# Optimization experiments

Hardware: AMD Instinct MI355X
Metric: run time of the kernel (lower is better)

The kernel has to match this reference:

```python
import jax, jax.numpy as jnp
import numpy as np

E = 4       # num_edge_types
DEPTH = 3   # args.depth (weight_tying=False -> DEPTH message layers)
V = 117     # num_atom_types


def setup_inputs() -> dict:
    key = jax.random.key(0)
    ks = jax.random.split(key, 13)
    mb, atoms, D, M = 1024, 128, 256, 512
    s = 0.05  # weight scale
    return {
        "atom_array": jax.random.randint(ks[0], (mb, atoms), 0, V),
        "adj": jax.random.uniform(ks[1], (mb, E, atoms, atoms), dtype=jnp.float32),
        "embed": jax.random.normal(ks[2], (V, D), jnp.float32) * s,
        "msg_W": jax.random.normal(ks[3], (DEPTH, E * D, D), jnp.float32) * s,
        "msg_b": jnp.zeros((DEPTH, E * D), jnp.float32),
        "W_ih": jax.random.normal(ks[4], (3 * D, D), jnp.float32) * s,
        "b_ih": jnp.zeros((3 * D,), jnp.float32),
        "W_hh": jax.random.normal(ks[5], (3 * D, D), jnp.float32) * s,
        "b_hh": jnp.zeros((3 * D,), jnp.float32),
        "i_W": jax.random.normal(ks[6], (M, 2 * D), jnp.float32) * s,
        "i_b": jnp.zeros((M,), jnp.float32),
        "j_W": jax.random.normal(ks[7], (M, D), jnp.float32) * s,
        "j_b": jnp.zeros((M,), jnp.float32),
    }


def _gru_cell(x, h, W_ih, b_ih, W_hh, b_hh):
    # PyTorch GRUCell math. x: input (message), h: hidden state.
    gi = x @ W_ih.T + b_ih
    gh = h @ W_hh.T + b_hh
    ir, iz, in_ = jnp.split(gi, 3, axis=-1)
    hr, hz, hn = jnp.split(gh, 3, axis=-1)
    r = jax.nn.sigmoid(ir + hr)
    z = jax.nn.sigmoid(iz + hz)
    n = jnp.tanh(in_ + r * hn)
    return (1.0 - z) * n + z * h


def reference(atom_array, adj, embed, msg_W, msg_b, W_ih, b_ih, W_hh, b_hh, i_W, i_b, j_W, j_b):
    mb, atoms = atom_array.shape
    D = embed.shape[1]
    h = embed[atom_array]          # [mb, atoms, D]
    h0 = h
    for step in range(DEPTH):
        # message: Linear(D -> E*D) then per-edge-type adjacency bmm, summed over edge types
        m = h @ msg_W[step].T + msg_b[step]            # [mb, atoms, E*D]
        m = m.reshape(mb, atoms, E, D).transpose(0, 2, 1, 3)  # [mb, E, atoms, D]
        m = jnp.einsum('beij,bejd->bid', adj, m)       # bmm + sum over edge types
        hid = h if step > 0 else jnp.zeros_like(h)     # GRUCell(hidden=None) at step 0
        h = _gru_cell(m, hid, W_ih, b_ih, W_hh, b_hh)  # [mb, atoms, D]
    # gated readout
    gate = jax.nn.sigmoid(jnp.concatenate([h, h0], axis=-1) @ i_W.T + i_b)  # [mb, atoms, M]
    val = h @ j_W.T + j_b                                                    # [mb, atoms, M]
    return jnp.sum(gate * val, axis=1)                                       # [mb, M]
```

## Files before the change

kernel.cpp:

```cpp
#include <hip/hip_runtime.h>
#include <cstdint>
#include <cstddef>

using f32x4 = float __attribute__((ext_vector_type(4)));
using u16x8 = unsigned short __attribute__((ext_vector_type(8)));
using u16x4 = unsigned short __attribute__((ext_vector_type(4)));
typedef _Float16 f16x8 __attribute__((ext_vector_type(8)));

#define DEV static __device__ __forceinline__

DEV unsigned short f2h(float f) {
  _Float16 x = (_Float16)f;
  return __builtin_bit_cast(unsigned short, x);
}
DEV float h2f(unsigned short s) {
  return (float)__builtin_bit_cast(_Float16, s);
}
DEV float sigm(float x) { return 1.f / (1.f + __expf(-x)); }
DEV float tanh_(float x) { return 2.f / (1.f + __expf(-2.f * x)) - 1.f; }

#define MFMA_F16(acc, va, vb) \
  acc = __builtin_amdgcn_mfma_f32_16x16x32_f16(va, vb, acc, 0, 0, 0)

constexpr int NB = 1024;
constexpr int AT = 128;
constexpr int DD = 256;
constexpr int MOUT = 512;
constexpr long NR = (long)NB * AT;

#define VWAIT(n) do { asm volatile("s_waitcnt vmcnt(" #n ")" ::: "memory"); \
                      __builtin_amdgcn_sched_barrier(0); } while (0)
#define LWAIT do { asm volatile("s_waitcnt lgkmcnt(0)" ::: "memory"); \
                   __builtin_amdgcn_sched_barrier(0); } while (0)
#define BARR do { __builtin_amdgcn_sched_barrier(0); __builtin_amdgcn_s_barrier(); \
                  __builtin_amdgcn_sched_barrier(0); } while (0)

#define XCD_SWZ(WG, N) const int WG = ((int)blockIdx.x & 7) * ((N) / 8) + ((int)blockIdx.x >> 3);

__global__ __launch_bounds__(256) void k_cvt(const float* __restrict__ src,
                                             unsigned short* __restrict__ dst) {
  long base = ((long)blockIdx.x * 256 + threadIdx.x) * 8;
  f32x4 v0 = *(const f32x4*)(src + base);
  f32x4 v1 = *(const f32x4*)(src + base + 4);
  u16x8 o;
  #pragma unroll
  for (int q = 0; q < 4; ++q) o[q] = f2h(v0[q]);
  #pragma unroll
  for (int q = 0; q < 4; ++q) o[4 + q] = f2h(v1[q]);
  *(u16x8*)(dst + base) = o;
}

__global__ __launch_bounds__(256) void k_cvt5(const float* __restrict__ s0, unsigned short* __restrict__ d0,
                                              const float* __restrict__ s1, unsigned short* __restrict__ d1,
                                              const float* __restrict__ s2, unsigned short* __restrict__ d2,
                                              const float* __restrict__ s3, unsigned short* __restrict__ d3,
                                              const float* __restrict__ s4, unsigned short* __restrict__ d4) {
  int blk = blockIdx.x;
  const float* s; unsigned short* d;
  if (blk < 384)      { s = s0; d = d0; }
  else if (blk < 480) { s = s1; d = d1; blk -= 384; }
  else if (blk < 576) { s = s2; d = d2; blk -= 480; }
  else if (blk < 704) { s = s3; d = d3; blk -= 576; }
  else                { s = s4; d = d4; blk -= 704; }
  long base = ((long)blk * 256 + threadIdx.x) * 8;
  f32x4 v0 = *(const f32x4*)(s + base);
  f32x4 v1 = *(const f32x4*)(s + base + 4);
  u16x8 o;
  #pragma unroll
  for (int q = 0; q < 4; ++q) o[q] = f2h(v0[q]);
  #pragma unroll
  for (int q = 0; q < 4; ++q) o[4 + q] = f2h(v1[q]);
  *(u16x8*)(d + base) = o;
}

__global__ __launch_bounds__(256) void k_gather(const int* __restrict__ atom,
                                                const float* __restrict__ embed,
                                                unsigned short* __restrict__ h,
                                                unsigned short* __restrict__ h0) {
  long idx = (long)blockIdx.x * 256 + threadIdx.x;
  long n = idx >> 6;
  int ch = (int)(idx & 63);
  int a = atom[n];
  f32x4 v = *(const f32x4*)(embed + (size_t)a * DD + ch * 4);
  u16x4 o;
  #pragma unroll
  for (int q = 0; q < 4; ++q) o[q] = f2h(v[q]);
  *(u16x4*)(h  + n * DD + ch * 4) = o;
  *(u16x4*)(h0 + n * DD + ch * 4) = o;
}

#define GEMM_IDS \
  const int tid = threadIdx.x, lane = tid & 63, wave = tid >> 6; \
  const int wr = wave >> 1, wc = wave & 1; \
  const int l15 = lane & 15, lg = lane >> 4; \
  const int sseg = (l15 >> 1) & 3;

#define GLDS(SRC, STRIDE, DST) \
  { \
    _Pragma("unroll") \
    for (int j_ = 0; j_ < 2; ++j_) { \
      const unsigned short* g_ = (SRC) + \
          (size_t)((wave * 2 + j_) * 16 + (lane >> 2)) * (STRIDE) + \
          ((lane & 3) ^ ((lane >> 3) & 3)) * 8; \
      __builtin_amdgcn_global_load_lds( \
          (const __attribute__((address_space(1))) void*)g_, \
          (__attribute__((address_space(3))) void*)&DST[(wave * 2 + j_) * 16][0], \
          16, 0, 0); \
    } \
  }

#define GLDS64(SRC, STRIDE, DST) \
  { \
    const unsigned short* g_ = (SRC) + \
        (size_t)(wave * 16 + (lane >> 2)) * (STRIDE) + \
        ((lane & 3) ^ ((lane >> 3) & 3)) * 8; \
    __builtin_amdgcn_global_load_lds( \
        (const __attribute__((address_space(1))) void*)g_, \
        (__attribute__((address_space(3))) void*)&DST[wave * 16][0], \
        16, 0, 0); \
  }

#define LOAD_A(AH) \
  f16x8 ah[4]; \
  _Pragma("unroll") \
  for (int m_ = 0; m_ < 4; ++m_) \
    ah[m_] = *(const f16x8*)&AH[wr * 64 + m_ * 16 + l15][(lg ^ sseg) * 8];

#define LOAD_B(BH) \
  f16x8 bh[4]; \
  _Pragma("unroll") \
  for (int n_ = 0; n_ < 4; ++n_) \
    bh[n_] = *(const f16x8*)&BH[wc * 64 + n_ * 16 + l15][(lg ^ sseg) * 8];

#define MFMA_TILE(ACC) \
  _Pragma("unroll") \
  for (int m_ = 0; m_ < 4; ++m_) \
    _Pragma("unroll") \
    for (int n_ = 0; n_ < 4; ++n_) \
      MFMA_F16(ACC[m_][n_], ah[m_], bh[n_]);

__global__ __launch_bounds__(256) void k_msgadj(const unsigned short* __restrict__ h,
                                                const unsigned short* __restrict__ W,
                                                const float* __restrict__ bias,
                                                const unsigned short* __restrict__ adjh,
                                                unsigned short* __restrict__ m_out) {
  __shared__ __align__(16) char pool[16384 + 128 * 136 * 2];
  typedef unsigned short row32[32];
  row32* As_[2] = { (row32*)pool,          (row32*)(pool + 16384) };
  row32* Bs_[2] = { (row32*)(pool + 8192), (row32*)(pool + 24576) };
  unsigned short (*PT)[136] = (unsigned short (*)[136])(pool + 16384);
  GEMM_IDS
  XCD_SWZ(wg, 2048)
  const size_t b = wg >> 1;
  const int d0 = (wg & 1) * 128;
  const unsigned short* hb = h + (size_t)b * 128 * 256;
  const unsigned short* adjb = adjh + (size_t)b * 4 * 128 * 128;
  f32x4 accM[4][4] = {};
  for (int e = 0; e < 4; ++e) {
    f32x4 accP[4][4] = {};
    const unsigned short* We = W + (size_t)(e * 256 + d0) * 256;
    const unsigned short* adje = adjb + (size_t)e * 128 * 128;
    GLDS(hb, 256, As_[0])
    GLDS(We, 256, Bs_[0])
    #pragma unroll
    for (int k0i = 0; k0i < 8; ++k0i) {
      const int cur = k0i & 1;
      if (k0i < 7) {
        row32* an_ = As_[cur ^ 1];
        row32* bn_ = Bs_[cur ^ 1];
        GLDS(hb + (k0i + 1) * 32, 256, an_)
        GLDS(We + (k0i + 1) * 32, 256, bn_)
      } else {
        GLDS(adje + 0 * 32, 128, As_[0])
        GLDS(adje + 1 * 32, 128, Bs_[0])
      }
      VWAIT(4);
      BARR;
      {
        row32* ac_ = As_[cur];
        row32* bc_ = Bs_[cur];
        LOAD_A(ac_)
        LOAD_B(bc_)
        MFMA_TILE(accP)
      }
      BARR;
    }
    #pragma unroll
    for (int m_ = 0; m_ < 4; ++m_) {
      int j0 = wr * 64 + m_ * 16 + lg * 4;
      #pragma unroll
      for (int n_ = 0; n_ < 4; ++n_) {
        int c = wc * 64 + n_ * 16 + l15;
        float bb = bias[e * 256 + d0 + c];
        u16x4 o;
        #pragma unroll
        for (int q = 0; q < 4; ++q) o[q] = f2h(accP[m_][n_][q] + bb);
        *(u16x4*)&PT[c][j0] = o;
      }
    }
    LWAIT;
    BARR;
    #pragma unroll
    for (int kt = 0; kt < 4; ++kt) {
      if (kt == 1) { GLDS(adje + 2 * 32, 128, As_[0]) }
      if (kt == 2) { GLDS(adje + 3 * 32, 128, Bs_[0]) }
      if (kt < 3) { VWAIT(2); } else { VWAIT(0); }
      BARR;
      {
        row32* ac_ = (kt & 1) ? Bs_[0] : As_[0];
        LOAD_A(ac_)
        f16x8 bh[4];
        #pragma unroll
        for (int n_ = 0; n_ < 4; ++n_)
          bh[n_] = *(const f16x8*)&PT[wc * 64 + n_ * 16 + l15][kt * 32 + lg * 8];
        MFMA_TILE(accM)
      }
      BARR;
    }
  }
  #pragma unroll
  for (int m_ = 0; m_ < 4; ++m_) {
    int i0 = wr * 64 + m_ * 16 + lg * 4;
    #pragma unroll
    for (int n_ = 0; n_ < 4; ++n_) {
      int c = d0 + wc * 64 + n_ * 16 + l15;
      #pragma unroll
      for (int q = 0; q < 4; ++q)
        m_out[((size_t)b * 128 + i0 + q) * 256 + c] = f2h(accM[m_][n_][q]);
    }
  }
}

template <bool HAS_H>
__global__ __launch_bounds__(256) void k_grufuse(const unsigned short* __restrict__ m,
                                                 const unsigned short* __restrict__ h,
                                                 const unsigned short* __restrict__ wih,
                                                 const unsigned short* __restrict__ whh,
                                                 const float* __restrict__ b_ih,
                                                 const float* __restrict__ b_hh,
                                                 unsigned short* __restrict__ h_new) {
  __shared__ unsigned short As[3][64][32];
  __shared__ unsigned short Br[3][64][32], Bz[3][64][32], Bn[3][64][32];
  GEMM_IDS
  XCD_SWZ(wg, 8192)
  const size_t b = wg >> 3;
  const int quad = wg & 7;
  const int r0 = (quad >> 2) * 64;
  const int c0 = (quad & 3) * 64;
  const unsigned short* msrc = m + ((size_t)b * 128 + r0) * 256;
  const unsigned short* hsrc = h + ((size_t)b * 128 + r0) * 256;
  constexpr int NKT = HAS_H ? 16 : 8;

  f32x4 accR[2][2] = {}, accZ[2][2] = {}, accI[2][2] = {}, accN[2][2] = {};

  auto stage = [&](int t, int s) {
    const unsigned short* a_ = ((HAS_H && t >= 8) ? hsrc : msrc) + (t & 7) * 32;
    const unsigned short* w_ = (HAS_H && t >= 8) ? whh : wih;
    GLDS64(a_, 256, As[s])
    GLDS64(w_ + (size_t)(c0) * 256 + (t & 7) * 32, 256, Br[s])
    GLDS64(w_ + (size_t)(256 + c0) * 256 + (t & 7) * 32, 256, Bz[s])
    GLDS64(w_ + (size_t)(512 + c0) * 256 + (t & 7) * 32, 256, Bn[s])
  };

  stage(0, 0);
  stage(1, 1);
  #pragma unroll
  for (int kt = 0; kt < NKT; ++kt) {
    const int cur = kt % 3;
    if (kt + 2 < NKT) stage(kt + 2, (kt + 2) % 3);
    if (kt + 2 < NKT) { VWAIT(8); } else if (kt + 2 == NKT) { VWAIT(4); } else { VWAIT(0); }
    BARR;
    f16x8 af[2], brf[2], bzf[2], bnf[2];
    #pragma unroll
    for (int m_ = 0; m_ < 2; ++m_)
      af[m_] = *(const f16x8*)&As[cur][wr * 32 + m_ * 16 + l15][(lg ^ sseg) * 8];
    #pragma unroll
    for (int n_ = 0; n_ < 2; ++n_) {
      brf[n_] = *(const f16x8*)&Br[cur][wc * 32 + n_ * 16 + l15][(lg ^ sseg) * 8];
      bzf[n_] = *(const f16x8*)&Bz[cur][wc * 32 + n_ * 16 + l15][(lg ^ sseg) * 8];
      bnf[n_] = *(const f16x8*)&Bn[cur][wc * 32 + n_ * 16 + l15][(lg ^ sseg) * 8];
    }
    #pragma unroll
    for (int m_ = 0; m_ < 2; ++m_)
      #pragma unroll
      for (int n_ = 0; n_ < 2; ++n_) {
        MFMA_F16(accR[m_][n_], af[m_], brf[n_]);
        MFMA_F16(accZ[m_][n_], af[m_], bzf[n_]);
        if (!HAS_H || kt < 8) { MFMA_F16(accI[m_][n_], af[m_], bnf[n_]); }
        else                  { MFMA_F16(accN[m_][n_], af[m_], bnf[n_]); }
      }
    BARR;
  }

  #pragma unroll
  for (int m_ = 0; m_ < 2; ++m_) {
    int rloc = r0 + wr * 32 + m_ * 16 + lg * 4;
    #pragma unroll
    for (int n_ = 0; n_ < 2; ++n_) {
      int c = c0 + wc * 32 + n_ * 16 + l15;
      float br = b_ih[c] + b_hh[c];
      float bz = b_ih[256 + c] + b_hh[256 + c];
      float bin = b_ih[512 + c], bhn = b_hh[512 + c];
      #pragma unroll
      for (int q = 0; q < 4; ++q) {
        size_t row = (size_t)b * 128 + rloc + q;
        float r = sigm(accR[m_][n_][q] + br);
        float z = sigm(accZ[m_][n_][q] + bz);
        float hn = (HAS_H ? accN[m_][n_][q] : 0.f) + bhn;
        float nn = tanh_(accI[m_][n_][q] + bin + r * hn);
        float hv = HAS_H ? h2f(h[row * 256 + c]) : 0.f;
        h_new[row * 256 + c] = f2h((1.f - z) * nn + z * hv);
      }
    }
  }
}

__global__ __launch_bounds__(256) void k_readout(const unsigned short* __restrict__ h,
                                                 const unsigned short* __restrict__ h0,
                                                 const unsigned short* __restrict__ iw,
                                                 const unsigned short* __restrict__ jw,
                                                 const float* __restrict__ ib,
                                                 const float* __restrict__ jb,
                                                 float* __restrict__ out) {
  __shared__ unsigned short As[2][128][32];
  __shared__ unsigned short Bg[2][128][32], Bv[2][128][32];
  __shared__ float red[2][128];
  GEMM_IDS
  XCD_SWZ(wg, 4096)
  const size_t b = wg >> 2;
  const int c0 = (wg & 3) * 128;
  auto as_src = [&](int t) {
    return (t < 8) ? (h + b * 128 * 256 + t * 32) : (h0 + b * 128 * 256 + (t - 8) * 32);
  };
  f32x4 accG[4][4] = {};
  f32x4 accV[4][4] = {};
  GLDS(as_src(0), 256, As[0])
  GLDS(iw + (size_t)c0 * 512, 512, Bg[0])
  GLDS(jw + (size_t)c0 * 256, 256, Bv[0])
  #pragma unroll
  for (int kt = 0; kt < 16; ++kt) {
    const int cur = kt & 1;
    if (kt + 1 < 16) {
      GLDS(as_src(kt + 1), 256, As[cur ^ 1])
      GLDS(iw + (size_t)c0 * 512 + (kt + 1) * 32, 512, Bg[cur ^ 1])
      if (kt + 1 < 8) GLDS(jw + (size_t)c0 * 256 + (kt + 1) * 32, 256, Bv[cur ^ 1])
    }
    if (kt < 7) { VWAIT(6); } else if (kt < 15) { VWAIT(4); } else { VWAIT(0); }
    BARR;
    LOAD_A(As[cur])
    f16x8 bg[4];
    #pragma unroll
    for (int n_ = 0; n_ < 4; ++n_)
      bg[n_] = *(const f16x8*)&Bg[cur][wc * 64 + n_ * 16 + l15][(lg ^ sseg) * 8];
    #pragma unroll
    for (int m_ = 0; m_ < 4; ++m_)
      #pragma unroll
      for (int n_ = 0; n_ < 4; ++n_)
        MFMA_F16(accG[m_][n_], ah[m_], bg[n_]);
    if (kt < 8) {
      f16x8 bv[4];
      #pragma unroll
      for (int n_ = 0; n_ < 4; ++n_)
        bv[n_] = *(const f16x8*)&Bv[cur][wc * 64 + n_ * 16 + l15][(lg ^ sseg) * 8];
      #pragma unroll
      for (int m_ = 0; m_ < 4; ++m_)
        #pragma unroll
        for (int n_ = 0; n_ < 4; ++n_)
          MFMA_F16(accV[m_][n_], ah[m_], bv[n_]);
    }
    BARR;
  }
  #pragma unroll
  for (int n_ = 0; n_ < 4; ++n_) {
    int c = c0 + wc * 64 + n_ * 16 + l15;
    float gb = ib[c], vb = jb[c];
    float s = 0.f;
    #pragma unroll
    for (int m_ = 0; m_ < 4; ++m_)
      #pragma unroll
      for (int q = 0; q < 4; ++q) {
        float g = sigm(accG[m_][n_][q] + gb);
        float v = accV[m_][n_][q] + vb;
        s += g * v;
      }
    s += __shfl_xor(s, 16);
    s += __shfl_xor(s, 32);
    if (lg == 0) red[wr][wc * 64 + n_ * 16 + l15] = s;
  }
  __syncthreads();
  if (tid < 128) out[b * MOUT + c0 + tid] = red[0][tid] + red[1][tid];
}

extern "C" void kernel_launch(void* const* d_in, const int* in_sizes, int n_in,
                              void* d_out, int out_size, void* d_ws, size_t ws_size,
                              hipStream_t stream) {
  const int*   atom  = (const int*)d_in[0];
  const float* adj   = (const float*)d_in[1];
  const float* embed = (const float*)d_in[2];
  const float* msg_W = (const float*)d_in[3];
  const float* msg_b = (const float*)d_in[4];
  const float* W_ih  = (const float*)d_in[5];
  const float* b_ih  = (const float*)d_in[6];
  const float* W_hh  = (const float*)d_in[7];
  const float* b_hh  = (const float*)d_in[8];
  const float* i_W   = (const float*)d_in[9];
  const float* i_b   = (const float*)d_in[10];
  const float* j_W   = (const float*)d_in[11];
  const float* j_b   = (const float*)d_in[12];
  float* out = (float*)d_out;

  const size_t SZ_H   = (size_t)NR * 256 * 2;
  const size_t SZ_ADJ = (size_t)NB * 4 * 128 * 128 * 2;

  char* p = (char*)d_ws;
  unsigned short* hA   = (unsigned short*)p;  p += SZ_H;
  unsigned short* hB   = (unsigned short*)p;  p += SZ_H;
  unsigned short* h0   = (unsigned short*)p;  p += SZ_H;
  unsigned short* m    = (unsigned short*)p;  p += SZ_H;
  unsigned short* adjh = (unsigned short*)p;  p += SZ_ADJ;
  unsigned short* wmsg = (unsigned short*)p;  p += (size_t)3 * 1024 * 256 * 2;
  unsigned short* wih  = (unsigned short*)p;  p += (size_t)768 * 256 * 2;
  unsigned short* whh  = (unsigned short*)p;  p += (size_t)768 * 256 * 2;
  unsigned short* wiw  = (unsigned short*)p;  p += (size_t)512 * 512 * 2;
  unsigned short* wjw  = (unsigned short*)p;  p += (size_t)512 * 256 * 2;
  if ((size_t)(p - (char*)d_ws) > ws_size) return;

  k_cvt<<<(int)((size_t)NB * 4 * 128 * 128 / 2048), 256, 0, stream>>>(adj, adjh);
  k_cvt5<<<768, 256, 0, stream>>>(msg_W, wmsg, W_ih, wih, W_hh, whh, i_W, wiw, j_W, wjw);

  k_gather<<<(int)(NR * 64 / 256), 256, 0, stream>>>(atom, embed, hA, h0);

  unsigned short* h_cur = hA;
  unsigned short* h_nxt = hB;
  for (int step = 0; step < 3; ++step) {
    k_msgadj<<<2048, 256, 0, stream>>>(h_cur, wmsg + (size_t)step * 262144,
                                       msg_b + (size_t)step * 1024, adjh, m);
    if (step == 0)
      k_grufuse<false><<<8192, 256, 0, stream>>>(m, h_cur, wih, whh, b_ih, b_hh, h_nxt);
    else
      k_grufuse<true><<<8192, 256, 0, stream>>>(m, h_cur, wih, whh, b_ih, b_hh, h_nxt);
    unsigned short* t = h_cur; h_cur = h_nxt; h_nxt = t;
  }

  k_readout<<<4096, 256, 0, stream>>>(h_cur, h0, wiw, wjw, i_b, j_b, out);
}
```

Baseline: 1.106 ms.

## Restructure GRU fused GEMM to process m and h K-tiles together, double-buffered

```diff
diff --git a/kernel.cpp b/kernel.cpp
--- a/kernel.cpp
+++ b/kernel.cpp
@@ -239,8 +239,9 @@
                                                  const float* __restrict__ b_ih,
                                                  const float* __restrict__ b_hh,
                                                  unsigned short* __restrict__ h_new) {
-  __shared__ unsigned short As[3][64][32];
-  __shared__ unsigned short Br[3][64][32], Bz[3][64][32], Bn[3][64][32];
+  __shared__ unsigned short Am[2][64][32], Ah[2][64][32];
+  __shared__ unsigned short Bri[2][64][32], Bzi[2][64][32], Bni[2][64][32];
+  __shared__ unsigned short Brh[2][64][32], Bzh[2][64][32], Bnh[2][64][32];
   GEMM_IDS
   XCD_SWZ(wg, 8192)
   const size_t b = wg >> 3;
@@ -249,46 +250,64 @@
   const int c0 = (quad & 3) * 64;
   const unsigned short* msrc = m + ((size_t)b * 128 + r0) * 256;
   const unsigned short* hsrc = h + ((size_t)b * 128 + r0) * 256;
-  constexpr int NKT = HAS_H ? 16 : 8;
 
   f32x4 accR[2][2] = {}, accZ[2][2] = {}, accI[2][2] = {}, accN[2][2] = {};
 
   auto stage = [&](int t, int s) {
-    const unsigned short* a_ = ((HAS_H && t >= 8) ? hsrc : msrc) + (t & 7) * 32;
-    const unsigned short* w_ = (HAS_H && t >= 8) ? whh : wih;
-    GLDS64(a_, 256, As[s])
-    GLDS64(w_ + (size_t)(c0) * 256 + (t & 7) * 32, 256, Br[s])
-    GLDS64(w_ + (size_t)(256 + c0) * 256 + (t & 7) * 32, 256, Bz[s])
-    GLDS64(w_ + (size_t)(512 + c0) * 256 + (t & 7) * 32, 256, Bn[s])
+    const int ko = t * 32;
+    GLDS64(msrc + ko, 256, Am[s])
+    GLDS64(wih + (size_t)(c0) * 256 + ko, 256, Bri[s])
+    GLDS64(wih + (size_t)(256 + c0) * 256 + ko, 256, Bzi[s])
+    GLDS64(wih + (size_t)(512 + c0) * 256 + ko, 256, Bni[s])
+    if (HAS_H) {
+      GLDS64(hsrc + ko, 256, Ah[s])
+      GLDS64(whh + (size_t)(c0) * 256 + ko, 256, Brh[s])
+      GLDS64(whh + (size_t)(256 + c0) * 256 + ko, 256, Bzh[s])
+      GLDS64(whh + (size_t)(512 + c0) * 256 + ko, 256, Bnh[s])
+    }
   };
 
   stage(0, 0);
-  stage(1, 1);
-  #pragma unroll
-  for (int kt = 0; kt < NKT; ++kt) {
-    const int cur = kt % 3;
-    if (kt + 2 < NKT) stage(kt + 2, (kt + 2) % 3);
-    if (kt + 2 < NKT) { VWAIT(8); } else if (kt + 2 == NKT) { VWAIT(4); } else { VWAIT(0); }
+  #pragma unroll
+  for (int kt = 0; kt < 8; ++kt) {
+    const int cur = kt & 1;
+    if (kt < 7) stage(kt + 1, cur ^ 1);
+    if (kt < 7) {
+      if constexpr (HAS_H) { VWAIT(8); } else { VWAIT(4); }
+    } else {
+      VWAIT(0);
+    }
     BARR;
-    f16x8 af[2], brf[2], bzf[2], bnf[2];
-    #pragma unroll
-    for (int m_ = 0; m_ < 2; ++m_)
-      af[m_] = *(const f16x8*)&As[cur][wr * 32 + m_ * 16 + l15][(lg ^ sseg) * 8];
+    f16x8 am_[2], ah_[2];
+    #pragma unroll
+    for (int m_ = 0; m_ < 2; ++m_) {
+      am_[m_] = *(const f16x8*)&Am[cur][wr * 32 + m_ * 16 + l15][(lg ^ sseg) * 8];
+      if (HAS_H)
+        ah_[m_] = *(const f16x8*)&Ah[cur][wr * 32 + m_ * 16 + l15][(lg ^ sseg) * 8];
+    }
     #pragma unroll
     for (int n_ = 0; n_ < 2; ++n_) {
-      brf[n_] = *(const f16x8*)&Br[cur][wc * 32 + n_ * 16 + l15][(lg ^ sseg) * 8];
-      bzf[n_] = *(const f16x8*)&Bz[cur][wc * 32 + n_ * 16 + l15][(lg ^ sseg) * 8];
-      bnf[n_] = *(const f16x8*)&Bn[cur][wc * 32 + n_ * 16 + l15][(lg ^ sseg) * 8];
-    }
-    #pragma unroll
-    for (int m_ = 0; m_ < 2; ++m_)
-      #pragma unroll
-      for (int n_ = 0; n_ < 2; ++n_) {
-        MFMA_F16(accR[m_][n_], af[m_], brf[n_]);
-        MFMA_F16(accZ[m_][n_], af[m_], bzf[n_]);
-        if (!HAS_H || kt < 8) { MFMA_F16(accI[m_][n_], af[m_], bnf[n_]); }
-        else                  { MFMA_F16(accN[m_][n_], af[m_], bnf[n_]); }
-      }
+      f16x8 bri = *(const f16x8*)&Bri[cur][wc * 32 + n_ * 16 + l15][(lg ^ sseg) * 8];
+      f16x8 bzi = *(const f16x8*)&Bzi[cur][wc * 32 + n_ * 16 + l15][(lg ^ sseg) * 8];
+      f16x8 bni = *(const f16x8*)&Bni[cur][wc * 32 + n_ * 16 + l15][(lg ^ sseg) * 8];
+      #pragma unroll
+      for (int m_ = 0; m_ < 2; ++m_) {
+        MFMA_F16(accR[m_][n_], am_[m_], bri);
+        MFMA_F16(accZ[m_][n_], am_[m_], bzi);
+        MFMA_F16(accI[m_][n_], am_[m_], bni);
+      }
+      if (HAS_H) {
+        f16x8 brh = *(const f16x8*)&Brh[cur][wc * 32 + n_ * 16 + l15][(lg ^ sseg) * 8];
+        f16x8 bzh = *(const f16x8*)&Bzh[cur][wc * 32 + n_ * 16 + l15][(lg ^ sseg) * 8];
+        f16x8 bnh = *(const f16x8*)&Bnh[cur][wc * 32 + n_ * 16 + l15][(lg ^ sseg) * 8];
+        #pragma unroll
+        for (int m_ = 0; m_ < 2; ++m_) {
+          MFMA_F16(accR[m_][n_], ah_[m_], brh);
+          MFMA_F16(accZ[m_][n_], ah_[m_], bzh);
+          MFMA_F16(accN[m_][n_], ah_[m_], bnh);
+        }
+      }
+    }
     BARR;
   }
 
```

After: 1.128 ms. About the same (+1.9%).

## Widen GRU kernel to 512-thread 128-row tiles with double-buffered staging

Applied to the files above, without the earlier changes.

```diff
diff --git a/kernel.cpp b/kernel.cpp
--- a/kernel.cpp
+++ b/kernel.cpp
@@ -117,6 +117,27 @@
     __builtin_amdgcn_global_load_lds( \
         (const __attribute__((address_space(1))) void*)g_, \
         (__attribute__((address_space(3))) void*)&DST[wave * 16][0], \
+        16, 0, 0); \
+  }
+
+#define GLDS128_8W(SRC, STRIDE, DST) \
+  { \
+    const unsigned short* g_ = (SRC) + \
+        (size_t)(wave * 16 + (lane >> 2)) * (STRIDE) + \
+        ((lane & 3) ^ ((lane >> 3) & 3)) * 8; \
+    __builtin_amdgcn_global_load_lds( \
+        (const __attribute__((address_space(1))) void*)g_, \
+        (__attribute__((address_space(3))) void*)&DST[wave * 16][0], \
+        16, 0, 0); \
+  }
+#define GLDS64_G(SRC, STRIDE, DST) \
+  { \
+    const unsigned short* g_ = (SRC) + \
+        (size_t)((wave & 3) * 16 + (lane >> 2)) * (STRIDE) + \
+        ((lane & 3) ^ ((lane >> 3) & 3)) * 8; \
+    __builtin_amdgcn_global_load_lds( \
+        (const __attribute__((address_space(1))) void*)g_, \
+        (__attribute__((address_space(3))) void*)&DST[(wave & 3) * 16][0], \
         16, 0, 0); \
   }
 
@@ -232,23 +253,21 @@
 }
 
 template <bool HAS_H>
-__global__ __launch_bounds__(256) void k_grufuse(const unsigned short* __restrict__ m,
+__global__ __launch_bounds__(512) void k_grufuse(const unsigned short* __restrict__ m,
                                                  const unsigned short* __restrict__ h,
                                                  const unsigned short* __restrict__ wih,
                                                  const unsigned short* __restrict__ whh,
                                                  const float* __restrict__ b_ih,
                                                  const float* __restrict__ b_hh,
                                                  unsigned short* __restrict__ h_new) {
-  __shared__ unsigned short As[3][64][32];
-  __shared__ unsigned short Br[3][64][32], Bz[3][64][32], Bn[3][64][32];
+  __shared__ unsigned short As[2][128][32];
+  __shared__ unsigned short Br[2][64][32], Bz[2][64][32], Bn[2][64][32];
   GEMM_IDS
-  XCD_SWZ(wg, 8192)
-  const size_t b = wg >> 3;
-  const int quad = wg & 7;
-  const int r0 = (quad >> 2) * 64;
-  const int c0 = (quad & 3) * 64;
-  const unsigned short* msrc = m + ((size_t)b * 128 + r0) * 256;
-  const unsigned short* hsrc = h + ((size_t)b * 128 + r0) * 256;
+  XCD_SWZ(wg, 4096)
+  const size_t b = wg >> 2;
+  const int c0 = (wg & 3) * 64;
+  const unsigned short* msrc = m + (size_t)b * 128 * 256;
+  const unsigned short* hsrc = h + (size_t)b * 128 * 256;
   constexpr int NKT = HAS_H ? 16 : 8;
 
   f32x4 accR[2][2] = {}, accZ[2][2] = {}, accI[2][2] = {}, accN[2][2] = {};
@@ -256,19 +275,25 @@
   auto stage = [&](int t, int s) {
     const unsigned short* a_ = ((HAS_H && t >= 8) ? hsrc : msrc) + (t & 7) * 32;
     const unsigned short* w_ = (HAS_H && t >= 8) ? whh : wih;
-    GLDS64(a_, 256, As[s])
-    GLDS64(w_ + (size_t)(c0) * 256 + (t & 7) * 32, 256, Br[s])
-    GLDS64(w_ + (size_t)(256 + c0) * 256 + (t & 7) * 32, 256, Bz[s])
-    GLDS64(w_ + (size_t)(512 + c0) * 256 + (t & 7) * 32, 256, Bn[s])
+    GLDS128_8W(a_, 256, As[s])
+    if (wave < 4) {
+      GLDS64_G(w_ + (size_t)(c0) * 256 + (t & 7) * 32, 256, Br[s])
+      GLDS64_G(w_ + (size_t)(512 + c0) * 256 + (t & 7) * 32, 256, Bn[s])
+    } else {
+      GLDS64_G(w_ + (size_t)(256 + c0) * 256 + (t & 7) * 32, 256, Bz[s])
+    }
   };
 
   stage(0, 0);
-  stage(1, 1);
   #pragma unroll
   for (int kt = 0; kt < NKT; ++kt) {
-    const int cur = kt % 3;
-    if (kt + 2 < NKT) stage(kt + 2, (kt + 2) % 3);
-    if (kt + 2 < NKT) { VWAIT(8); } else if (kt + 2 == NKT) { VWAIT(4); } else { VWAIT(0); }
+    const int cur = kt & 1;
+    if (kt + 1 < NKT) stage(kt + 1, cur ^ 1);
+    if (kt + 1 < NKT) {
+      if (wave < 4) { VWAIT(3); } else { VWAIT(2); }
+    } else {
+      VWAIT(0);
+    }
     BARR;
     f16x8 af[2], brf[2], bzf[2], bnf[2];
     #pragma unroll
@@ -294,7 +319,7 @@
 
   #pragma unroll
   for (int m_ = 0; m_ < 2; ++m_) {
-    int rloc = r0 + wr * 32 + m_ * 16 + lg * 4;
+    int rloc = wr * 32 + m_ * 16 + lg * 4;
     #pragma unroll
     for (int n_ = 0; n_ < 2; ++n_) {
       int c = c0 + wc * 32 + n_ * 16 + l15;
@@ -436,9 +461,9 @@
     k_msgadj<<<2048, 256, 0, stream>>>(h_cur, wmsg + (size_t)step * 262144,
                                        msg_b + (size_t)step * 1024, adjh, m);
     if (step == 0)
-      k_grufuse<false><<<8192, 256, 0, stream>>>(m, h_cur, wih, whh, b_ih, b_hh, h_nxt);
+      k_grufuse<false><<<4096, 512, 0, stream>>>(m, h_cur, wih, whh, b_ih, b_hh, h_nxt);
     else
-      k_grufuse<true><<<8192, 256, 0, stream>>>(m, h_cur, wih, whh, b_ih, b_hh, h_nxt);
+      k_grufuse<true><<<4096, 512, 0, stream>>>(m, h_cur, wih, whh, b_ih, b_hh, h_nxt);
     unsigned short* t = h_cur; h_cur = h_nxt; h_nxt = t;
   }
 
```

New measurement: 1.137 ms. 2.7% more time.

## Load GRU GEMM operands directly from global into registers, dropping LDS staging

Applied to the files above, without the earlier changes.

```diff
diff --git a/kernel.cpp b/kernel.cpp
--- a/kernel.cpp
+++ b/kernel.cpp
@@ -107,17 +107,6 @@
           (__attribute__((address_space(3))) void*)&DST[(wave * 2 + j_) * 16][0], \
           16, 0, 0); \
     } \
-  }
-
-#define GLDS64(SRC, STRIDE, DST) \
-  { \
-    const unsigned short* g_ = (SRC) + \
-        (size_t)(wave * 16 + (lane >> 2)) * (STRIDE) + \
-        ((lane & 3) ^ ((lane >> 3) & 3)) * 8; \
-    __builtin_amdgcn_global_load_lds( \
-        (const __attribute__((address_space(1))) void*)g_, \
-        (__attribute__((address_space(3))) void*)&DST[wave * 16][0], \
-        16, 0, 0); \
   }
 
 #define LOAD_A(AH) \
@@ -239,57 +228,55 @@
                                                  const float* __restrict__ b_ih,
                                                  const float* __restrict__ b_hh,
                                                  unsigned short* __restrict__ h_new) {
-  __shared__ unsigned short As[3][64][32];
-  __shared__ unsigned short Br[3][64][32], Bz[3][64][32], Bn[3][64][32];
-  GEMM_IDS
+  const int tid = threadIdx.x, lane = tid & 63, wave = tid >> 6;
+  const int wr = wave >> 1, wc = wave & 1;
+  const int l15 = lane & 15, lg = lane >> 4;
   XCD_SWZ(wg, 8192)
   const size_t b = wg >> 3;
   const int quad = wg & 7;
   const int r0 = (quad >> 2) * 64;
   const int c0 = (quad & 3) * 64;
-  const unsigned short* msrc = m + ((size_t)b * 128 + r0) * 256;
-  const unsigned short* hsrc = h + ((size_t)b * 128 + r0) * 256;
+
+  const unsigned short* msrc = m + ((size_t)b * 128 + r0 + wr * 32 + l15) * 256 + lg * 8;
+  const unsigned short* hsrc = h + ((size_t)b * 128 + r0 + wr * 32 + l15) * 256 + lg * 8;
+  const size_t bofs = (size_t)(c0 + wc * 32 + l15) * 256 + lg * 8;
+  const unsigned short* wi = wih + bofs;
+  const unsigned short* wh = whh + bofs;
+
   constexpr int NKT = HAS_H ? 16 : 8;
-
   f32x4 accR[2][2] = {}, accZ[2][2] = {}, accI[2][2] = {}, accN[2][2] = {};
 
-  auto stage = [&](int t, int s) {
-    const unsigned short* a_ = ((HAS_H && t >= 8) ? hsrc : msrc) + (t & 7) * 32;
-    const unsigned short* w_ = (HAS_H && t >= 8) ? whh : wih;
-    GLDS64(a_, 256, As[s])
-    GLDS64(w_ + (size_t)(c0) * 256 + (t & 7) * 32, 256, Br[s])
-    GLDS64(w_ + (size_t)(256 + c0) * 256 + (t & 7) * 32, 256, Bz[s])
-    GLDS64(w_ + (size_t)(512 + c0) * 256 + (t & 7) * 32, 256, Bn[s])
+  f16x8 a_[2][2], br_[2][2], bz_[2][2], bn_[2][2];
+
+  auto load_tile = [&](int t, int s) {
+    const unsigned short* A = (HAS_H && t >= 8) ? hsrc : msrc;
+    const unsigned short* W = (HAS_H && t >= 8) ? wh : wi;
+    const int ko = (t & 7) * 32;
+    #pragma unroll
+    for (int m_ = 0; m_ < 2; ++m_)
+      a_[s][m_] = *(const f16x8*)(A + (size_t)(m_ * 16) * 256 + ko);
+    #pragma unroll
+    for (int n_ = 0; n_ < 2; ++n_) {
+      br_[s][n_] = *(const f16x8*)(W + (size_t)(0 * 256 + n_ * 16) * 256 + ko);
+      bz_[s][n_] = *(const f16x8*)(W + (size_t)(1 * 256 + n_ * 16) * 256 + ko);
+      bn_[s][n_] = *(const f16x8*)(W + (size_t)(2 * 256 + n_ * 16) * 256 + ko);
+    }
   };
 
-  stage(0, 0);
-  stage(1, 1);
+  load_tile(0, 0);
   #pragma unroll
   for (int kt = 0; kt < NKT; ++kt) {
-    const int cur = kt % 3;
-    if (kt + 2 < NKT) stage(kt + 2, (kt + 2) % 3);
-    if (kt + 2 < NKT) { VWAIT(8); } else if (kt + 2 == NKT) { VWAIT(4); } else { VWAIT(0); }
-    BARR;
-    f16x8 af[2], brf[2], bzf[2], bnf[2];
+    const int cur = kt & 1;
+    if (kt + 1 < NKT) load_tile(kt + 1, cur ^ 1);
     #pragma unroll
     for (int m_ = 0; m_ < 2; ++m_)
-      af[m_] = *(const f16x8*)&As[cur][wr * 32 + m_ * 16 + l15][(lg ^ sseg) * 8];
-    #pragma unroll
-    for (int n_ = 0; n_ < 2; ++n_) {
-      brf[n_] = *(const f16x8*)&Br[cur][wc * 32 + n_ * 16 + l15][(lg ^ sseg) * 8];
-      bzf[n_] = *(const f16x8*)&Bz[cur][wc * 32 + n_ * 16 + l15][(lg ^ sseg) * 8];
-      bnf[n_] = *(const f16x8*)&Bn[cur][wc * 32 + n_ * 16 + l15][(lg ^ sseg) * 8];
-    }
-    #pragma unroll
-    for (int m_ = 0; m_ < 2; ++m_)
       #pragma unroll
       for (int n_ = 0; n_ < 2; ++n_) {
-        MFMA_F16(accR[m_][n_], af[m_], brf[n_]);
-        MFMA_F16(accZ[m_][n_], af[m_], bzf[n_]);
-        if (!HAS_H || kt < 8) { MFMA_F16(accI[m_][n_], af[m_], bnf[n_]); }
-        else                  { MFMA_F16(accN[m_][n_], af[m_], bnf[n_]); }
-      }
-    BARR;
+        MFMA_F16(accR[m_][n_], a_[cur][m_], br_[cur][n_]);
+        MFMA_F16(accZ[m_][n_], a_[cur][m_], bz_[cur][n_]);
+        if (!HAS_H || kt < 8) { MFMA_F16(accI[m_][n_], a_[cur][m_], bn_[cur][n_]); }
+        else                  { MFMA_F16(accN[m_][n_], a_[cur][m_], bn_[cur][n_]); }
+      }
   }
 
   #pragma unroll
```

New measurement: 1.845 ms. 1.67x slower.
